# Kernel optimization log

Hardware: AMD Instinct MI355X
Metric: run time of the kernel (lower is better)

The kernel has to match this reference:

```python
import jax, jax.numpy as jnp
import numpy as np

VOCAB = 256
D = 256      # FLAGS.duration_lstm_dim
B = 32
L = 2048


def setup_inputs() -> dict:
    key = jax.random.key(0)
    ks = jax.random.split(key, 8)
    s = 0.05
    return {
        "phonemes": jax.random.randint(ks[0], (B, L), 0, VOCAB),
        "lengths": jax.random.randint(ks[1], (B,), 0, L),
        "embed_table": jax.random.normal(ks[2], (VOCAB, D), jnp.float32) * s,
        "w_fwd": jax.random.normal(ks[3], (2 * D, 4 * D), jnp.float32) * s,
        "b_fwd": jnp.zeros((4 * D,), jnp.float32),
        "w_bwd": jax.random.normal(ks[4], (2 * D, 4 * D), jnp.float32) * s,
        "b_bwd": jnp.zeros((4 * D,), jnp.float32),
        "w_proj": jax.random.normal(ks[5], (2 * D, 1), jnp.float32) * s,
        "b_proj": jnp.zeros((1,), jnp.float32),
    }


def lstm_unroll(x, w, b, reset=None):
    """Haiku-style LSTM unrolled over time (batch-major x: [B,L,D]).

    w: [(D_in + D_h), 4*D_h] acting on concat([x, h]); gate order i,g,f,o
    with forget bias +1 (matches hk.LSTM). If `reset` ([B,L] bool) is given,
    state is reset to zeros where True BEFORE each step (hk.ResetCore).
    """
    Bn, Ln, d = x.shape
    wx, wh = w[:d], w[d:]
    # Batch the input->gates matmul over all timesteps (same math as per-step).
    xg = jnp.swapaxes(x @ wx + b, 0, 1)  # [L, B, 4D] time-major
    if reset is None:
        reset_t = jnp.zeros((Ln, Bn), dtype=bool)
    else:
        reset_t = jnp.swapaxes(reset, 0, 1)  # [L, B]

    def step(carry, inp):
        h, c = carry
        xg_t, r_t = inp
        r = r_t[:, None]
        h = jnp.where(r, 0.0, h)
        c = jnp.where(r, 0.0, c)
        gates = xg_t + h @ wh
        i, g, f, o = jnp.split(gates, 4, axis=-1)
        c = jax.nn.sigmoid(f + 1.0) * c + jax.nn.sigmoid(i) * jnp.tanh(g)
        h = jax.nn.sigmoid(o) * jnp.tanh(c)
        return (h, c), h

    init = (jnp.zeros((Bn, d), x.dtype), jnp.zeros((Bn, d), x.dtype))
    _, hs = jax.lax.scan(step, init, (xg, reset_t))
    return jnp.swapaxes(hs, 0, 1)  # [B, L, D]


def reference(phonemes, lengths, embed_table, w_fwd, b_fwd, w_bwd, b_bwd,
              w_proj, b_proj):
    x = embed_table[phonemes]                      # [B, L, D]
    Ln = x.shape[1]
    mask = jnp.arange(Ln)[None, :] < (lengths[:, None] - 1)  # [B, L]
    # forward LSTM
    h_fwd = lstm_unroll(x, w_fwd, b_fwd)
    # backward LSTM with ResetCore on flipped inputs/mask
    x_bwd = jnp.flip(x, axis=1)
    mask_bwd = jnp.flip(mask, axis=1)
    h_bwd = lstm_unroll(x_bwd, w_bwd, b_bwd, reset=mask_bwd)
    y = jnp.concatenate([h_fwd, jnp.flip(h_bwd, axis=1)], axis=-1)  # [B,L,2D]
    return jax.nn.relu(y @ w_proj + b_proj)        # [B, L, 1]
```

## Files before the change

### kernel.cpp

```cpp
#include <hip/hip_runtime.h>
#include <math.h>

#define VOCAB 256
#define DD    256
#define BB    32
#define LL    2048
#define G4    1024
#define NB    16
#define TPB   512

typedef __attribute__((ext_vector_type(8))) short short8;
typedef __attribute__((ext_vector_type(4))) float floatx4;

__device__ __forceinline__ float sigf(float x) { return 1.0f / (1.0f + __expf(-x)); }

__device__ __forceinline__ unsigned short f2bf(float x) {
    unsigned u = __builtin_bit_cast(unsigned, x);
    u = u + 0x7fffu + ((u >> 16) & 1u);
    return (unsigned short)(u >> 16);
}
__device__ __forceinline__ float bf2f(unsigned short b) {
    unsigned u = ((unsigned)b) << 16;
    return __builtin_bit_cast(float, u);
}

__global__ __launch_bounds__(256) void k_table(
    const float* __restrict__ embed,
    const float* __restrict__ w_fwd, const float* __restrict__ b_fwd,
    const float* __restrict__ w_bwd, const float* __restrict__ b_bwd,
    float* __restrict__ tbl)
{
    const int dir = blockIdx.x >> 8;
    const int v   = blockIdx.x & 255;
    const float* __restrict__ w    = dir ? w_bwd : w_fwd;
    const float* __restrict__ bias = dir ? b_bwd : b_fwd;

    __shared__ __align__(16) float e[DD];
    const int tid = threadIdx.x;
    e[tid] = embed[v * DD + tid];
    __syncthreads();

    const float4* __restrict__ wx4 = (const float4*)w;
    float4 acc = ((const float4*)bias)[tid];
    #pragma unroll 2
    for (int k = 0; k < DD; k += 4) {
        float4 h4 = *(const float4*)&e[k];
        float4 w0 = wx4[(size_t)(k + 0) * 256 + tid];
        float4 w1 = wx4[(size_t)(k + 1) * 256 + tid];
        float4 w2 = wx4[(size_t)(k + 2) * 256 + tid];
        float4 w3 = wx4[(size_t)(k + 3) * 256 + tid];
        acc.x += h4.x * w0.x + h4.y * w1.x + h4.z * w2.x + h4.w * w3.x;
        acc.y += h4.x * w0.y + h4.y * w1.y + h4.z * w2.y + h4.w * w3.y;
        acc.z += h4.x * w0.z + h4.y * w1.z + h4.z * w2.z + h4.w * w3.z;
        acc.w += h4.x * w0.w + h4.y * w1.w + h4.z * w2.w + h4.w * w3.w;
    }
    ((float4*)tbl)[((size_t)dir * VOCAB + v) * 256 + tid] = acc;
}

__global__ void k_zero(int* __restrict__ ctr) {
    ctr[threadIdx.x] = 0;
}

__global__ __launch_bounds__(TPB, 2) void k_scan_b(
    const int*   __restrict__ ph,
    const int*   __restrict__ lens,
    const float* __restrict__ w_fwd,
    const float* __restrict__ w_bwd,
    const float* __restrict__ w_proj,
    const float* __restrict__ tbl,
    unsigned*    __restrict__ Hpk_all,
    float* __restrict__ pp,
    int*   __restrict__ ctr)
{
    const int dir  = blockIdx.x >> 4;
    const int j    = blockIdx.x & (NB - 1);
    const int tid  = threadIdx.x;
    const int lane = tid & 63;
    const int wv   = tid >> 6;
    const int mt   = wv >> 2;
    const int gt   = wv & 3;

    const float* __restrict__ Wh = (dir ? w_bwd : w_fwd) + (size_t)DD * G4;
    const float* __restrict__ tb = tbl + (size_t)dir * VOCAB * G4;
    unsigned* __restrict__ Hpk = Hpk_all + (size_t)dir * 2 * BB * DD;
    int* ctrd = ctr + dir * 32;

    __shared__ unsigned short Ahi[BB * DD];
    __shared__ unsigned short Alo[BB * DD];
    __shared__ float gl[4][BB][17];
    const int b     = tid >> 4;
    const int dd    = tid & 15;
    const int dglob = j * 16 + dd;
    float c = 0.0f;
    const int   lenb = lens[b];
    const float wpd  = w_proj[dir * DD + dglob];

    short8 bhi[8], blo[8];
    {
        const int ccol  = gt * DD + j * 16 + (lane & 15);
        const int krow0 = 8 * (lane >> 4);
        #pragma unroll
        for (int kk = 0; kk < 8; ++kk) {
            short8 th, tl;
            #pragma unroll
            for (int e = 0; e < 8; ++e) {
                float wval = Wh[(size_t)(kk * 32 + krow0 + e) * G4 + ccol];
                unsigned short hi = f2bf(wval);
                th[e] = (short)hi;
                tl[e] = (short)f2bf(wval - bf2f(hi));
            }
            bhi[kk] = th;
            blo[kk] = tl;
        }
    }

    float xg0, xg1, xg2, xg3;
    {
        const int t0 = dir ? (LL - 1) : 0;
        const int v  = ph[b * LL + t0];
        const float* __restrict__ trow = tb + (size_t)v * G4 + dglob;
        xg0 = trow[0]; xg1 = trow[DD]; xg2 = trow[2 * DD]; xg3 = trow[3 * DD];
    }

    for (int s = 0; s < LL; ++s) {
        const int t = dir ? (LL - 1 - s) : s;

        if (s) {
            if (tid == 0) {
                const int target = NB * s;
                int guard = 0;
                while (__hip_atomic_load(ctrd, __ATOMIC_RELAXED, __HIP_MEMORY_SCOPE_AGENT) < target) {
                    __builtin_amdgcn_s_sleep(1);
                    if (++guard > 200000000) break;
                }
            }
            __syncthreads();

            {
                const int r = tid >> 4;
                const int o = (tid & 15) * 16;
                const bool rz = (dir != 0) && (t < lenb - 1);
                unsigned long long u[8];
                unsigned long long* src = (unsigned long long*)
                    (Hpk + ((s & 1) ^ 1) * (BB * DD) + r * DD + o);
                #pragma unroll
                for (int e = 0; e < 8; ++e)
                    u[e] = __hip_atomic_load(src + e, __ATOMIC_RELAXED, __HIP_MEMORY_SCOPE_AGENT);
                if (rz) {
                    #pragma unroll
                    for (int e = 0; e < 8; ++e) u[e] = 0ull;
                }
                #pragma unroll
                for (int hchunk = 0; hchunk < 2; ++hchunk) {
                    short8 sh, sl;
                    #pragma unroll
                    for (int e = 0; e < 4; ++e) {
                        const unsigned long long ue = u[4 * hchunk + e];
                        const unsigned lo32 = (unsigned)ue;
                        const unsigned hi32 = (unsigned)(ue >> 32);
                        sh[2 * e]     = (short)(lo32 >> 16);
                        sl[2 * e]     = (short)(lo32 & 0xffffu);
                        sh[2 * e + 1] = (short)(hi32 >> 16);
                        sl[2 * e + 1] = (short)(hi32 & 0xffffu);
                    }
                    const int k8   = (o >> 3) + hchunk;
                    const int byte = ((r * 32 + k8) << 4) ^ ((r & 7) << 4);
                    *(short8*)((char*)Ahi + byte) = sh;
                    *(short8*)((char*)Alo + byte) = sl;
                }
            }
            __syncthreads();

            {
                floatx4 acc = {0.f, 0.f, 0.f, 0.f};
                const int row = mt * 16 + (lane & 15);
                const int swz = (row & 7) << 4;
                const int k8b = lane >> 4;
                #pragma unroll
                for (int kk = 0; kk < 8; ++kk) {
                    const int byte = ((row * 32 + kk * 4 + k8b) << 4) ^ swz;
                    short8 ah = *(const short8*)((const char*)Ahi + byte);
                    short8 al = *(const short8*)((const char*)Alo + byte);
                    acc = __builtin_amdgcn_mfma_f32_16x16x32_bf16(ah, bhi[kk], acc, 0, 0, 0);
                    acc = __builtin_amdgcn_mfma_f32_16x16x32_bf16(al, bhi[kk], acc, 0, 0, 0);
                    acc = __builtin_amdgcn_mfma_f32_16x16x32_bf16(ah, blo[kk], acc, 0, 0, 0);
                }
                const int bl = mt * 16 + (lane >> 4) * 4;
                #pragma unroll
                for (int r2 = 0; r2 < 4; ++r2) gl[gt][bl + r2][lane & 15] = acc[r2];
            }
            __syncthreads();
        }

        float h;
        {
            float xi  = xg0;
            float xgg = xg1;
            float xf  = xg2;
            float xo  = xg3;
            if (s) {
                xi  += gl[0][b][dd];
                xgg += gl[1][b][dd];
                xf  += gl[2][b][dd];
                xo  += gl[3][b][dd];
            }
            if (dir && (t < lenb - 1)) c = 0.0f;
            c = sigf(xf + 1.0f) * c + sigf(xi) * tanhf(xgg);
            h = sigf(xo) * tanhf(c);
            const unsigned short hhi = f2bf(h);
            const unsigned short hlo = f2bf(h - bf2f(hhi));
            const unsigned upk = ((unsigned)hhi << 16) | (unsigned)hlo;
            __hip_atomic_store(Hpk + (s & 1) * (BB * DD) + b * DD + dglob, upk,
                               __ATOMIC_RELAXED, __HIP_MEMORY_SCOPE_AGENT);
        }
        __syncthreads();
        if (tid == 0)
            __hip_atomic_fetch_add(ctrd, 1, __ATOMIC_RELAXED, __HIP_MEMORY_SCOPE_AGENT);

        {
            float pr = h * wpd;
            pr += __shfl_xor(pr, 1, 16);
            pr += __shfl_xor(pr, 2, 16);
            pr += __shfl_xor(pr, 4, 16);
            pr += __shfl_xor(pr, 8, 16);
            if (dd == 0) pp[((size_t)(dir * NB + j) * BB + b) * LL + t] = pr;
        }
        if (s + 1 < LL) {
            const int tn = dir ? (LL - 2 - s) : (s + 1);
            const int v  = ph[b * LL + tn];
            const float* __restrict__ trow = tb + (size_t)v * G4 + dglob;
            xg0 = trow[0]; xg1 = trow[DD]; xg2 = trow[2 * DD]; xg3 = trow[3 * DD];
        }
    }
}

__global__ __launch_bounds__(256) void k_comb(
    const float* __restrict__ pp,
    const float* __restrict__ b_proj,
    float* __restrict__ out)
{
    const int i = blockIdx.x * 256 + threadIdx.x;
    float sv = b_proj[0];
    #pragma unroll
    for (int q = 0; q < 2 * NB; ++q) sv += pp[(size_t)q * (BB * LL) + i];
    out[i] = sv > 0.0f ? sv : 0.0f;
}

extern "C" void kernel_launch(void* const* d_in, const int* in_sizes, int n_in,
                              void* d_out, int out_size, void* d_ws, size_t ws_size,
                              hipStream_t stream)
{
    const int*   phon = (const int*)d_in[0];
    const int*   lens = (const int*)d_in[1];
    const float* emb  = (const float*)d_in[2];
    const float* wf   = (const float*)d_in[3];
    const float* bf   = (const float*)d_in[4];
    const float* wb   = (const float*)d_in[5];
    const float* bbi  = (const float*)d_in[6];
    const float* wp   = (const float*)d_in[7];
    const float* bp   = (const float*)d_in[8];
    float* out = (float*)d_out;

    float*    ws  = (float*)d_ws;
    float*    tbl = ws;
    float*    pp  = tbl + 2 * VOCAB * G4;
    unsigned* Hpk = (unsigned*)(pp + (size_t)2 * NB * BB * LL);
    int*      ctr = (int*)(Hpk + 2 * 2 * BB * DD);

    k_zero  <<<1, 64, 0, stream>>>(ctr);
    k_table <<<2 * VOCAB, 256, 0, stream>>>(emb, wf, bf, wb, bbi, tbl);
    k_scan_b<<<2 * NB, TPB, 0, stream>>>(phon, lens, wf, wb, wp, tbl, Hpk, pp, ctr);
    k_comb  <<<(BB * LL) / 256, 256, 0, stream>>>(pp, bp, out);
}
```

Measured before the change: 8.002 ms.

## Replace global step counter barrier with per-element step-tagged hidden state flags

Drops the shared atomic step counter and the block-wide spin-wait by packing a step tag into the upper 32 bits of each 64-bit hidden-state word. Each thread polls only the 16 entries it needs until they carry the expected tag. This removes a syncthreads and a serialized tid-0 poll per timestep, along with the k_zero launch. In exchange it doubles the bytes exchanged per step and relies on stale workspace tags never matching. Rows under reset skip the wait entirely, which could let a block run ahead of its peers.

```diff
diff --git a/kernel.cpp b/kernel.cpp
--- a/kernel.cpp
+++ b/kernel.cpp
@@ -57,20 +57,15 @@
     ((float4*)tbl)[((size_t)dir * VOCAB + v) * 256 + tid] = acc;
 }
 
-__global__ void k_zero(int* __restrict__ ctr) {
-    ctr[threadIdx.x] = 0;
-}
-
-__global__ __launch_bounds__(TPB, 2) void k_scan_b(
+__global__ __launch_bounds__(TPB) void k_scan_b(
     const int*   __restrict__ ph,
     const int*   __restrict__ lens,
     const float* __restrict__ w_fwd,
     const float* __restrict__ w_bwd,
     const float* __restrict__ w_proj,
     const float* __restrict__ tbl,
-    unsigned*    __restrict__ Hpk_all,
-    float* __restrict__ pp,
-    int*   __restrict__ ctr)
+    unsigned long long* __restrict__ Hpk_all,
+    float* __restrict__ pp)
 {
     const int dir  = blockIdx.x >> 4;
     const int j    = blockIdx.x & (NB - 1);
@@ -82,18 +77,21 @@
 
     const float* __restrict__ Wh = (dir ? w_bwd : w_fwd) + (size_t)DD * G4;
     const float* __restrict__ tb = tbl + (size_t)dir * VOCAB * G4;
-    unsigned* __restrict__ Hpk = Hpk_all + (size_t)dir * 2 * BB * DD;
-    int* ctrd = ctr + dir * 32;
+    unsigned long long* __restrict__ Hd = Hpk_all + (size_t)dir * 2 * BB * DD;
 
     __shared__ unsigned short Ahi[BB * DD];
     __shared__ unsigned short Alo[BB * DD];
     __shared__ float gl[4][BB][17];
+
     const int b     = tid >> 4;
     const int dd    = tid & 15;
     const int dglob = j * 16 + dd;
     float c = 0.0f;
     const int   lenb = lens[b];
     const float wpd  = w_proj[dir * DD + dglob];
+
+    const int r = tid >> 4;
+    const int o = (tid & 15) * 16;
 
     short8 bhi[8], blo[8];
     {
@@ -126,42 +124,44 @@
         const int t = dir ? (LL - 1 - s) : s;
 
         if (s) {
-            if (tid == 0) {
-                const int target = NB * s;
-                int guard = 0;
-                while (__hip_atomic_load(ctrd, __ATOMIC_RELAXED, __HIP_MEMORY_SCOPE_AGENT) < target) {
-                    __builtin_amdgcn_s_sleep(1);
-                    if (++guard > 200000000) break;
-                }
-            }
-            __syncthreads();
-
             {
-                const int r = tid >> 4;
-                const int o = (tid & 15) * 16;
                 const bool rz = (dir != 0) && (t < lenb - 1);
-                unsigned long long u[8];
-                unsigned long long* src = (unsigned long long*)
-                    (Hpk + ((s & 1) ^ 1) * (BB * DD) + r * DD + o);
-                #pragma unroll
-                for (int e = 0; e < 8; ++e)
-                    u[e] = __hip_atomic_load(src + e, __ATOMIC_RELAXED, __HIP_MEMORY_SCOPE_AGENT);
-                if (rz) {
+                unsigned pay[16];
+                if (!rz) {
+                    unsigned long long* __restrict__ src =
+                        Hd + ((s & 1) ^ 1) * (BB * DD) + r * DD + o;
+                    const unsigned tag = (unsigned)s;
+                    unsigned pend = 0xFFFFu;
+                    int guard = 0;
+                    while (pend) {
+                        #pragma unroll
+                        for (int e = 0; e < 16; ++e) {
+                            if (pend & (1u << e)) {
+                                unsigned long long ue = __hip_atomic_load(
+                                    src + e, __ATOMIC_RELAXED, __HIP_MEMORY_SCOPE_AGENT);
+                                if ((unsigned)(ue >> 32) == tag) {
+                                    pay[e] = (unsigned)ue;
+                                    pend &= ~(1u << e);
+                                }
+                            }
+                        }
+                        if (pend) {
+                            __builtin_amdgcn_s_sleep(1);
+                            if (++guard > 50000000) break;
+                        }
+                    }
+                } else {
                     #pragma unroll
-                    for (int e = 0; e < 8; ++e) u[e] = 0ull;
+                    for (int e = 0; e < 16; ++e) pay[e] = 0u;
                 }
                 #pragma unroll
                 for (int hchunk = 0; hchunk < 2; ++hchunk) {
                     short8 sh, sl;
                     #pragma unroll
-                    for (int e = 0; e < 4; ++e) {
-                        const unsigned long long ue = u[4 * hchunk + e];
-                        const unsigned lo32 = (unsigned)ue;
-                        const unsigned hi32 = (unsigned)(ue >> 32);
-                        sh[2 * e]     = (short)(lo32 >> 16);
-                        sl[2 * e]     = (short)(lo32 & 0xffffu);
-                        sh[2 * e + 1] = (short)(hi32 >> 16);
-                        sl[2 * e + 1] = (short)(hi32 & 0xffffu);
+                    for (int e = 0; e < 8; ++e) {
+                        const unsigned p = pay[8 * hchunk + e];
+                        sh[e] = (short)(p >> 16);
+                        sl[e] = (short)(p & 0xffffu);
                     }
                     const int k8   = (o >> 3) + hchunk;
                     const int byte = ((r * 32 + k8) << 4) ^ ((r & 7) << 4);
@@ -209,13 +209,12 @@
             h = sigf(xo) * tanhf(c);
             const unsigned short hhi = f2bf(h);
             const unsigned short hlo = f2bf(h - bf2f(hhi));
-            const unsigned upk = ((unsigned)hhi << 16) | (unsigned)hlo;
-            __hip_atomic_store(Hpk + (s & 1) * (BB * DD) + b * DD + dglob, upk,
+            const unsigned long long upk =
+                ((unsigned long long)(unsigned)(s + 1) << 32) |
+                (unsigned long long)(((unsigned)hhi << 16) | (unsigned)hlo);
+            __hip_atomic_store(Hd + (s & 1) * (BB * DD) + b * DD + dglob, upk,
                                __ATOMIC_RELAXED, __HIP_MEMORY_SCOPE_AGENT);
         }
-        __syncthreads();
-        if (tid == 0)
-            __hip_atomic_fetch_add(ctrd, 1, __ATOMIC_RELAXED, __HIP_MEMORY_SCOPE_AGENT);
 
         {
             float pr = h * wpd;
@@ -261,14 +260,13 @@
     const float* bp   = (const float*)d_in[8];
     float* out = (float*)d_out;
 
-    float*    ws  = (float*)d_ws;
-    float*    tbl = ws;
-    float*    pp  = tbl + 2 * VOCAB * G4;
-    unsigned* Hpk = (unsigned*)(pp + (size_t)2 * NB * BB * LL);
-    int*      ctr = (int*)(Hpk + 2 * 2 * BB * DD);
-
-    k_zero  <<<1, 64, 0, stream>>>(ctr);
+    float* ws  = (float*)d_ws;
+    float* tbl = ws;
+    float* pp  = tbl + 2 * VOCAB * G4;
+    unsigned long long* Hpk =
+        (unsigned long long*)(pp + (size_t)2 * NB * BB * LL);
+
     k_table <<<2 * VOCAB, 256, 0, stream>>>(emb, wf, bf, wb, bbi, tbl);
-    k_scan_b<<<2 * NB, TPB, 0, stream>>>(phon, lens, wf, wb, wp, tbl, Hpk, pp, ctr);
+    k_scan_b<<<2 * NB, TPB, 0, stream>>>(phon, lens, wf, wb, wp, tbl, Hpk, pp);
     k_comb  <<<(BB * LL) / 256, 256, 0, stream>>>(pp, bp, out);
 }
```

After: 12.06 ms. 1.51x slower.
